# Kernel optimization log

Hardware: AMD Instinct MI355X
Metric: run time of the kernel (lower is better)

## Reference

```python
import jax, jax.numpy as jnp
import numpy as np

N = 32768      # total nodes
E = 524288     # edges (avg degree 16)
HID = 256      # hidden_dim
H = 8          # heads
C = HID // H   # head dim = 32
G = 64         # graphs in batch
NPG = N // G   # nodes per graph = 512
EDIM = 2       # edge feature dim
NEG_SLOPE = 0.2  # PyG GATv2 default


def setup_inputs():
    key = jax.random.key(0)
    ks = jax.random.split(key, 12)
    s = 0.05
    return dict(
        x=jax.random.normal(ks[0], (N, HID), jnp.float32),
        edge_attr=jax.random.normal(ks[1], (E, EDIM), jnp.float32),
        # GATv2Conv params
        W_l=jax.random.normal(ks[2], (HID, HID), jnp.float32) * s,
        b_l=jnp.zeros((HID,), jnp.float32),
        W_r=jax.random.normal(ks[3], (HID, HID), jnp.float32) * s,
        b_r=jnp.zeros((HID,), jnp.float32),
        W_e=jax.random.normal(ks[4], (EDIM, HID), jnp.float32) * s,
        att=jax.random.normal(ks[5], (H, C), jnp.float32) * s,
        bias_gat=jnp.zeros((HID,), jnp.float32),
        # MultiheadAttention params (torch packed qkv layout)
        in_proj_w=jax.random.normal(ks[6], (3 * HID, HID), jnp.float32) * s,
        in_proj_b=jnp.zeros((3 * HID,), jnp.float32),
        out_proj_w=jax.random.normal(ks[7], (HID, HID), jnp.float32) * s,
        out_proj_b=jnp.zeros((HID,), jnp.float32),
        alpha_param=jnp.array(0.5, jnp.float32),
        # FFN
        W1=jax.random.normal(ks[8], (HID, 4 * HID), jnp.float32) * s,
        b1=jnp.zeros((4 * HID,), jnp.float32),
        W2=jax.random.normal(ks[9], (4 * HID, HID), jnp.float32) * s,
        b2=jnp.zeros((HID,), jnp.float32),
        # LayerNorms
        g1=jnp.ones((HID,), jnp.float32), be1=jnp.zeros((HID,), jnp.float32),
        g2=jnp.ones((HID,), jnp.float32), be2=jnp.zeros((HID,), jnp.float32),
        g3=jnp.ones((HID,), jnp.float32), be3=jnp.zeros((HID,), jnp.float32),
        edge_index=jax.random.randint(ks[10], (2, E), 0, N, jnp.int32),
        batch=jnp.repeat(jnp.arange(G, dtype=jnp.int32), NPG),
    )


def _ln(x, g, b, eps=1e-5):
    m = jnp.mean(x, -1, keepdims=True)
    v = jnp.mean((x - m) ** 2, -1, keepdims=True)
    return (x - m) * jax.lax.rsqrt(v + eps) * g + b


def _gatv2(x, edge_index, edge_attr, W_l, b_l, W_r, b_r, W_e, att, bias_gat):
    src, dst = edge_index[0], edge_index[1]
    # PyG add_self_loops with fill_value='mean': self-loop edge_attr at node i
    # is the mean of edge_attr over edges incoming to i (0 if none).
    deg = jax.ops.segment_sum(jnp.ones((E,), x.dtype), dst, num_segments=N)
    ea_mean = jax.ops.segment_sum(edge_attr, dst, num_segments=N) / jnp.maximum(deg, 1.0)[:, None]
    loop = jnp.arange(N, dtype=src.dtype)
    src2 = jnp.concatenate([src, loop])
    dst2 = jnp.concatenate([dst, loop])
    ea2 = jnp.concatenate([edge_attr, ea_mean], axis=0)  # [E+N, 2]
    xl = (x @ W_l + b_l).reshape(N, H, C)  # source transform (messages)
    xr = (x @ W_r + b_r).reshape(N, H, C)  # target transform
    ee = (ea2 @ W_e).reshape(-1, H, C)
    e = jax.nn.leaky_relu(xl[src2] + xr[dst2] + ee, NEG_SLOPE)  # [E+N, H, C]
    score = jnp.einsum('ehc,hc->eh', e, att)  # [E+N, H]
    # scatter softmax over incoming edges of each target node
    smax = jax.lax.stop_gradient(jax.ops.segment_max(score, dst2, num_segments=N))
    ex = jnp.exp(score - smax[dst2])
    ssum = jax.ops.segment_sum(ex, dst2, num_segments=N)
    alpha = ex / ssum[dst2]  # [E+N, H]
    out = jax.ops.segment_sum(alpha[:, :, None] * xl[src2], dst2, num_segments=N)
    return out.reshape(N, HID) + bias_gat


def _mha(xg, in_proj_w, in_proj_b, out_proj_w, out_proj_b):
    # xg: [G, NPG, HID]; torch nn.MultiheadAttention (batch_first, eval mode)
    qkv = xg @ in_proj_w.T + in_proj_b
    q, k, v = jnp.split(qkv, 3, axis=-1)
    q = q.reshape(G, NPG, H, C)
    k = k.reshape(G, NPG, H, C)
    v = v.reshape(G, NPG, H, C)
    scores = jnp.einsum('gqhd,gkhd->ghqk', q, k) / jnp.sqrt(jnp.float32(C))
    p = jax.nn.softmax(scores, axis=-1)
    o = jnp.einsum('ghqk,gkhd->gqhd', p, v).reshape(G, NPG, HID)
    return o @ out_proj_w.T + out_proj_b


def reference(x, edge_attr, W_l, b_l, W_r, b_r, W_e, att, bias_gat,
              in_proj_w, in_proj_b, out_proj_w, out_proj_b, alpha_param,
              W1, b1, W2, b2, g1, be1, g2, be2, g3, be3, edge_index, batch):
    local_out = _ln(
        _gatv2(x, edge_index, edge_attr, W_l, b_l, W_r, b_r, W_e, att, bias_gat),
        g1, be1)
    # batch is sorted with equal-sized graphs -> the per-graph ragged
    # attention loop equals one batched [G, NPG, NPG] attention
    xg = x.reshape(G, NPG, HID)
    global_out = _mha(xg, in_proj_w, in_proj_b, out_proj_w, out_proj_b).reshape(N, HID)
    global_out = _ln(global_out, g2, be2)
    a = jax.nn.sigmoid(alpha_param)
    combined = a * local_out + (1.0 - a) * global_out
    ffn = jax.nn.gelu(combined @ W1 + b1, approximate=False) @ W2 + b2
    return _ln(combined + ffn, g3, be3)
```

## Files before the change

kernel.cpp:

```cpp
#include <hip/hip_runtime.h>
#include <math.h>

#define N_NODES 32768
#define E_EDGES 524288
#define HIDDEN  256
#define NPG     512
#define NGRAPH  64
#define NHEAD   8
#define CDIM    32

typedef unsigned short bf16;
typedef __attribute__((ext_vector_type(8))) short short8;
typedef __attribute__((ext_vector_type(4))) float f4;

__device__ inline float bf2f(unsigned short u) {
    union { unsigned int i; float f; } v; v.i = ((unsigned int)u) << 16; return v.f;
}
__device__ inline unsigned short f2bf(float f) {
    union { float f; unsigned int i; } v; v.f = f;
    unsigned int x = v.i;
    return (unsigned short)((x + 0x7FFFu + ((x >> 16) & 1u)) >> 16);
}
__device__ inline float4 load4(const float* p) { return *(const float4*)p; }
__device__ inline float4 load4(const bf16* p) {
    ushort4 u = *(const ushort4*)p;
    return make_float4(bf2f(u.x), bf2f(u.y), bf2f(u.z), bf2f(u.w));
}
__device__ inline void store4(float* p, float4 v) { *(float4*)p = v; }
__device__ inline void store4(bf16* p, float4 v) {
    ushort4 u; u.x = f2bf(v.x); u.y = f2bf(v.y); u.z = f2bf(v.z); u.w = f2bf(v.w);
    *(ushort4*)p = u;
}


__global__ void zero_kernel(float* deg, float* ea_sum, int* fill) {
    int i = blockIdx.x * blockDim.x + threadIdx.x;
    if (i < 2 * N_NODES) ea_sum[i] = 0.0f;
    if (i < N_NODES) { deg[i] = 0.0f; fill[i] = 0; }
}

__global__ void deg_kernel(const int* __restrict__ ei, const float* __restrict__ edge_attr,
                           float* deg, float* ea_sum) {
    int e = blockIdx.x * blockDim.x + threadIdx.x;
    if (e >= E_EDGES) return;
    int d = ei[E_EDGES + e];
    atomicAdd(&deg[d], 1.0f);
    atomicAdd(&ea_sum[2 * d + 0], edge_attr[2 * e + 0]);
    atomicAdd(&ea_sum[2 * d + 1], edge_attr[2 * e + 1]);
}

__global__ void eamean_kernel(const float* __restrict__ deg, float* ea_mean) {
    int i = blockIdx.x * blockDim.x + threadIdx.x;
    if (i >= N_NODES) return;
    float dm = fmaxf(deg[i], 1.0f);
    ea_mean[2 * i + 0] /= dm;
    ea_mean[2 * i + 1] /= dm;
}

__global__ __launch_bounds__(1024) void scan_kernel(const float* __restrict__ deg, int* row_ptr) {
    __shared__ int part[1024];
    int t = threadIdx.x;
    int base = t * 32;
    int loc[32];
    int s = 0;
    #pragma unroll
    for (int j = 0; j < 32; j++) {
        loc[j] = s;
        s += (int)deg[base + j] + 1;
    }
    int mysum = s;
    part[t] = s;
    __syncthreads();
    for (int off = 1; off < 1024; off <<= 1) {
        int v = 0;
        if (t >= off) v = part[t - off];
        __syncthreads();
        part[t] += v;
        __syncthreads();
    }
    int offset = part[t] - mysum;
    #pragma unroll
    for (int j = 0; j < 32; j++) row_ptr[base + j] = offset + loc[j];
    if (t == 1023) row_ptr[N_NODES] = part[1023];
}

__global__ void fill_kernel(const int* __restrict__ ei, const int* __restrict__ row_ptr,
                            int* fill, int* col) {
    int tid = blockIdx.x * blockDim.x + threadIdx.x;
    if (tid >= E_EDGES + N_NODES) return;
    int d;
    if (tid < E_EDGES) d = ei[E_EDGES + tid];
    else               d = tid - E_EDGES;
    int pos = row_ptr[d] + atomicAdd(&fill[d], 1);
    col[pos] = tid;
}

__global__ void convw_t(const float* __restrict__ src, bf16* __restrict__ dst, int K, int N) {
    int i = blockIdx.x * 256 + threadIdx.x;
    if (i >= K * N) return;
    int k = i / N, n = i - k * N;
    dst[n * K + k] = f2bf(src[i]);
}
__global__ void convv(const float* __restrict__ src, bf16* __restrict__ dst, int total4) {
    int i = blockIdx.x * 256 + threadIdx.x;
    if (i >= total4) return;
    float4 v = *(const float4*)&src[i * 4];
    store4(&dst[i * 4], v);
}

template <int EPI>
__global__ __launch_bounds__(256) void mfma_gemm(
    const bf16* __restrict__ A, const bf16* __restrict__ Wb,
    const float* __restrict__ bias, const bf16* __restrict__ res,
    bf16* __restrict__ C, int M, int N, int K)
{
    __shared__ bf16 lds[2 * 128 * 72];
    bf16* As = lds;
    bf16* Bs = lds + 128 * 72;
    int tid = threadIdx.x;
    int wave = tid >> 6, lane = tid & 63;
    int quad = lane >> 4, l16 = lane & 15;
    int n0 = blockIdx.x * 128, m0 = blockIdx.y * 128;
    int wm = (wave & 1) * 64, wn = (wave >> 1) * 64;

    f4 acc[4][4] = {};

    for (int k0 = 0; k0 < K; k0 += 64) {
        #pragma unroll
        for (int i = 0; i < 4; i++) {
            int idx = i * 256 + tid;
            int row = idx >> 3, kc = (idx & 7) * 8;
            *(int4*)&As[row * 72 + kc] = *(const int4*)&A[(size_t)(m0 + row) * K + k0 + kc];
            *(int4*)&Bs[row * 72 + kc] = *(const int4*)&Wb[(size_t)(n0 + row) * K + k0 + kc];
        }
        __syncthreads();
        #pragma unroll
        for (int ks = 0; ks < 2; ks++) {
            short8 af[4], bfr[4];
            #pragma unroll
            for (int mt = 0; mt < 4; mt++)
                af[mt] = *(const short8*)&As[(wm + mt * 16 + l16) * 72 + ks * 32 + quad * 8];
            #pragma unroll
            for (int nt = 0; nt < 4; nt++)
                bfr[nt] = *(const short8*)&Bs[(wn + nt * 16 + l16) * 72 + ks * 32 + quad * 8];
            #pragma unroll
            for (int mt = 0; mt < 4; mt++)
                #pragma unroll
                for (int nt = 0; nt < 4; nt++)
                    acc[mt][nt] = __builtin_amdgcn_mfma_f32_16x16x32_bf16(
                        af[mt], bfr[nt], acc[mt][nt], 0, 0, 0);
        }
        __syncthreads();
    }

    float* epi = (float*)lds + wave * 16 * 68;
    int row = lane >> 2;
    int cb = (lane & 3) * 16;
    int gn = n0 + wn + cb;
    float bb[16];
    *(float4*)&bb[0]  = *(const float4*)&bias[gn + 0];
    *(float4*)&bb[4]  = *(const float4*)&bias[gn + 4];
    *(float4*)&bb[8]  = *(const float4*)&bias[gn + 8];
    *(float4*)&bb[12] = *(const float4*)&bias[gn + 12];

    for (int mt = 0; mt < 4; mt++) {
        #pragma unroll
        for (int nt = 0; nt < 4; nt++)
            #pragma unroll
            for (int r = 0; r < 4; r++)
                epi[(quad * 4 + r) * 68 + nt * 16 + l16] = acc[mt][nt][r];
        float vv[16];
        *(float4*)&vv[0]  = *(float4*)&epi[row * 68 + cb + 0];
        *(float4*)&vv[4]  = *(float4*)&epi[row * 68 + cb + 4];
        *(float4*)&vv[8]  = *(float4*)&epi[row * 68 + cb + 8];
        *(float4*)&vv[12] = *(float4*)&epi[row * 68 + cb + 12];
        int gm = m0 + wm + mt * 16 + row;
        #pragma unroll
        for (int j = 0; j < 16; j++) vv[j] += bb[j];
        if (EPI == 1) {
            #pragma unroll
            for (int j = 0; j < 16; j++)
                vv[j] = 0.5f * vv[j] * (1.0f + erff(vv[j] * 0.70710678118654752f));
        } else if (EPI == 2) {
            ushort rr[16];
            const bf16* rp = &res[(size_t)gm * N + gn];
            *(int4*)&rr[0] = *(const int4*)&rp[0];
            *(int4*)&rr[8] = *(const int4*)&rp[8];
            #pragma unroll
            for (int j = 0; j < 16; j++) vv[j] += bf2f(rr[j]);
        }
        ushort o16[16];
        #pragma unroll
        for (int j = 0; j < 16; j++) o16[j] = f2bf(vv[j]);
        bf16* cp = &C[(size_t)gm * N + gn];
        *(int4*)&cp[0] = *(int4*)&o16[0];
        *(int4*)&cp[8] = *(int4*)&o16[8];
    }
}

__global__ __launch_bounds__(256) void attn_mfma(
    const bf16* __restrict__ qkv, bf16* __restrict__ attnout)
{
    __shared__ bf16 Ks[128 * 40];
    __shared__ bf16 Vt[32 * 136];
    __shared__ bf16 Pb[4 * 64 * 40];

    int b = blockIdx.x;
    int g = b >> 4, h = (b >> 1) & 7, hlf = b & 1;
    int tid = threadIdx.x;
    int wave = tid >> 6, lane = tid & 63;
    int quad = lane >> 4, l16 = lane & 15;
    int qbase = hlf * 256 + wave * 64;
    bf16* Pw = &Pb[wave * 64 * 40];
    const float SCALE = 0.17677669529663687f;

    short8 qf[4];
    #pragma unroll
    for (int mt = 0; mt < 4; mt++) {
        size_t node = (size_t)(g * NPG + qbase + mt * 16 + l16);
        qf[mt] = *(const short8*)&qkv[node * 768 + h * CDIM + quad * 8];
    }

    f4 oacc[4][2] = {};
    float lacc[4][4] = {};

    for (int c = 0; c < 4; c++) {
        int kk0 = c * 128;
        __syncthreads();
        #pragma unroll
        for (int i = 0; i < 2; i++) {
            int idx = i * 256 + tid;
            int key = idx >> 2, kc = (idx & 3) * 8;
            *(int4*)&Ks[key * 40 + kc] =
                *(const int4*)&qkv[(size_t)(g * NPG + kk0 + key) * 768 + 256 + h * CDIM + kc];
        }
        {
            int key = tid >> 1, dblk = (tid & 1) * 16;
            ushort tmp[16];
            const bf16* vp = &qkv[(size_t)(g * NPG + kk0 + key) * 768 + 512 + h * CDIM + dblk];
            *(int4*)&tmp[0] = *(const int4*)&vp[0];
            *(int4*)&tmp[8] = *(const int4*)&vp[8];
            #pragma unroll
            for (int j = 0; j < 16; j++) Vt[(dblk + j) * 136 + key] = tmp[j];
        }
        __syncthreads();

        for (int sub = 0; sub < 4; sub++) {
            int ks0 = sub * 32;
            short8 kf[2];
            #pragma unroll
            for (int nt = 0; nt < 2; nt++)
                kf[nt] = *(const short8*)&Ks[(ks0 + nt * 16 + l16) * 40 + quad * 8];
            #pragma unroll
            for (int mt = 0; mt < 4; mt++) {
                #pragma unroll
                for (int nt = 0; nt < 2; nt++) {
                    f4 z = {0.f, 0.f, 0.f, 0.f};
                    f4 s = __builtin_amdgcn_mfma_f32_16x16x32_bf16(qf[mt], kf[nt], z, 0, 0, 0);
                    #pragma unroll
                    for (int r = 0; r < 4; r++) {
                        float p = __expf(s[r] * SCALE);
                        lacc[mt][r] += p;
                        Pw[(mt * 16 + quad * 4 + r) * 40 + nt * 16 + l16] = f2bf(p);
                    }
                }
            }
            short8 vf[2];
            #pragma unroll
            for (int dt = 0; dt < 2; dt++)
                vf[dt] = *(const short8*)&Vt[(dt * 16 + l16) * 136 + ks0 + quad * 8];
            #pragma unroll
            for (int mt = 0; mt < 4; mt++) {
                short8 pf = *(const short8*)&Pw[(mt * 16 + l16) * 40 + quad * 8];
                #pragma unroll
                for (int dt = 0; dt < 2; dt++)
                    oacc[mt][dt] = __builtin_amdgcn_mfma_f32_16x16x32_bf16(
                        pf, vf[dt], oacc[mt][dt], 0, 0, 0);
            }
        }
    }

    #pragma unroll
    for (int mt = 0; mt < 4; mt++)
        #pragma unroll
        for (int r = 0; r < 4; r++) {
            float l = lacc[mt][r];
            l += __shfl_xor(l, 1);
            l += __shfl_xor(l, 2);
            l += __shfl_xor(l, 4);
            l += __shfl_xor(l, 8);
            lacc[mt][r] = l;
        }

    #pragma unroll
    for (int mt = 0; mt < 4; mt++) {
        #pragma unroll
        for (int dt = 0; dt < 2; dt++) {
            #pragma unroll
            for (int r = 0; r < 4; r++) {
                float v = oacc[mt][dt][r] / lacc[mt][r];
                size_t node = (size_t)(g * NPG + qbase + mt * 16 + quad * 4 + r);
                attnout[node * HIDDEN + h * CDIM + dt * 16 + l16] = f2bf(v);
            }
        }
    }
}

__global__ __launch_bounds__(256) void gat_kernel(
    const bf16* __restrict__ xl, const bf16* __restrict__ xr,
    const int* __restrict__ row_ptr, const int* __restrict__ col,
    const int* __restrict__ ei, const float* __restrict__ edge_attr,
    const float* __restrict__ ea_mean,
    const float* __restrict__ W_e, const float* __restrict__ att,
    const float* __restrict__ bias_gat,
    const float* __restrict__ g1, const float* __restrict__ be1,
    bf16* __restrict__ out)
{
    int wave = threadIdx.x >> 6;
    int lane = threadIdx.x & 63;
    int node = blockIdx.x * 4 + wave;
    int cb = lane * 4;

    float4 xr4 = load4(&xr[(size_t)node * HIDDEN + cb]);
    float4 we0 = *(const float4*)&W_e[cb];
    float4 we1 = *(const float4*)&W_e[HIDDEN + cb];
    float4 at4 = *(const float4*)&att[cb];

    int rs = row_ptr[node], re = row_ptr[node + 1];
    float lsum = 0.0f;
    float acc0 = 0.f, acc1 = 0.f, acc2 = 0.f, acc3 = 0.f;

    for (int idx = rs; idx < re; idx++) {
        int eid = col[idx];
        int s; float ea0, ea1;
        if (eid < E_EDGES) {
            s = ei[eid];
            ea0 = edge_attr[2 * eid + 0];
            ea1 = edge_attr[2 * eid + 1];
        } else {
            s = node;
            ea0 = ea_mean[2 * node + 0];
            ea1 = ea_mean[2 * node + 1];
        }
        float4 xl4 = load4(&xl[(size_t)s * HIDDEN + cb]);
        float t, p = 0.0f;
        t = xl4.x + xr4.x + ea0 * we0.x + ea1 * we1.x; t = (t > 0.f) ? t : 0.2f * t; p += t * at4.x;
        t = xl4.y + xr4.y + ea0 * we0.y + ea1 * we1.y; t = (t > 0.f) ? t : 0.2f * t; p += t * at4.y;
        t = xl4.z + xr4.z + ea0 * we0.z + ea1 * we1.z; t = (t > 0.f) ? t : 0.2f * t; p += t * at4.z;
        t = xl4.w + xr4.w + ea0 * we0.w + ea1 * we1.w; t = (t > 0.f) ? t : 0.2f * t; p += t * at4.w;
        p += __shfl_xor(p, 1);
        p += __shfl_xor(p, 2);
        p += __shfl_xor(p, 4);
        float w = __expf(p);
        lsum += w;
        acc0 += w * xl4.x; acc1 += w * xl4.y; acc2 += w * xl4.z; acc3 += w * xl4.w;
    }
    float inv = 1.0f / lsum;
    float v0 = acc0 * inv + bias_gat[cb + 0];
    float v1 = acc1 * inv + bias_gat[cb + 1];
    float v2 = acc2 * inv + bias_gat[cb + 2];
    float v3 = acc3 * inv + bias_gat[cb + 3];

    float s = v0 + v1 + v2 + v3;
    #pragma unroll
    for (int m = 1; m < 64; m <<= 1) s += __shfl_xor(s, m);
    float mean = s * (1.0f / 256.0f);
    float d0 = v0 - mean, d1 = v1 - mean, d2 = v2 - mean, d3 = v3 - mean;
    float sq = d0 * d0 + d1 * d1 + d2 * d2 + d3 * d3;
    #pragma unroll
    for (int m = 1; m < 64; m <<= 1) sq += __shfl_xor(sq, m);
    float rstd = rsqrtf(sq * (1.0f / 256.0f) + 1e-5f);
    float4 o;
    o.x = d0 * rstd * g1[cb + 0] + be1[cb + 0];
    o.y = d1 * rstd * g1[cb + 1] + be1[cb + 1];
    o.z = d2 * rstd * g1[cb + 2] + be1[cb + 2];
    o.w = d3 * rstd * g1[cb + 3] + be1[cb + 3];
    store4(&out[(size_t)node * HIDDEN + cb], o);
}

__global__ __launch_bounds__(256) void combine_kernel(
    const bf16* __restrict__ gout, const bf16* __restrict__ localout,
    const float* __restrict__ alpha_p,
    const float* __restrict__ g2, const float* __restrict__ be2,
    bf16* __restrict__ combined)
{
    int wave = threadIdx.x >> 6;
    int lane = threadIdx.x & 63;
    int node = blockIdx.x * 4 + wave;
    int cb = lane * 4;
    float4 gv = load4(&gout[(size_t)node * HIDDEN + cb]);
    float s = gv.x + gv.y + gv.z + gv.w;
    #pragma unroll
    for (int m = 1; m < 64; m <<= 1) s += __shfl_xor(s, m);
    float mean = s * (1.0f / 256.0f);
    float d0 = gv.x - mean, d1 = gv.y - mean, d2 = gv.z - mean, d3 = gv.w - mean;
    float sq = d0 * d0 + d1 * d1 + d2 * d2 + d3 * d3;
    #pragma unroll
    for (int m = 1; m < 64; m <<= 1) sq += __shfl_xor(sq, m);
    float rstd = rsqrtf(sq * (1.0f / 256.0f) + 1e-5f);
    float n0 = d0 * rstd * g2[cb + 0] + be2[cb + 0];
    float n1 = d1 * rstd * g2[cb + 1] + be2[cb + 1];
    float n2 = d2 * rstd * g2[cb + 2] + be2[cb + 2];
    float n3 = d3 * rstd * g2[cb + 3] + be2[cb + 3];
    float a = 1.0f / (1.0f + __expf(-alpha_p[0]));
    float4 lv = load4(&localout[(size_t)node * HIDDEN + cb]);
    float4 o;
    o.x = a * lv.x + (1.0f - a) * n0;
    o.y = a * lv.y + (1.0f - a) * n1;
    o.z = a * lv.z + (1.0f - a) * n2;
    o.w = a * lv.w + (1.0f - a) * n3;
    store4(&combined[(size_t)node * HIDDEN + cb], o);
}

__global__ __launch_bounds__(256) void finalln_kernel(
    const bf16* __restrict__ ffn,
    const float* __restrict__ g3, const float* __restrict__ be3,
    float* __restrict__ out)
{
    int wave = threadIdx.x >> 6;
    int lane = threadIdx.x & 63;
    int node = blockIdx.x * 4 + wave;
    int cb = lane * 4;
    float4 v = load4(&ffn[(size_t)node * HIDDEN + cb]);
    float s = v.x + v.y + v.z + v.w;
    #pragma unroll
    for (int m = 1; m < 64; m <<= 1) s += __shfl_xor(s, m);
    float mean = s * (1.0f / 256.0f);
    float d0 = v.x - mean, d1 = v.y - mean, d2 = v.z - mean, d3 = v.w - mean;
    float sq = d0 * d0 + d1 * d1 + d2 * d2 + d3 * d3;
    #pragma unroll
    for (int m = 1; m < 64; m <<= 1) sq += __shfl_xor(sq, m);
    float rstd = rsqrtf(sq * (1.0f / 256.0f) + 1e-5f);
    float4 o;
    o.x = d0 * rstd * g3[cb + 0] + be3[cb + 0];
    o.y = d1 * rstd * g3[cb + 1] + be3[cb + 1];
    o.z = d2 * rstd * g3[cb + 2] + be3[cb + 2];
    o.w = d3 * rstd * g3[cb + 3] + be3[cb + 3];
    *(float4*)&out[(size_t)node * HIDDEN + cb] = o;
}

extern "C" void kernel_launch(void* const* d_in, const int* in_sizes, int n_in,
                              void* d_out, int out_size, void* d_ws, size_t ws_size,
                              hipStream_t stream) {
    const float* x          = (const float*)d_in[0];
    const float* edge_attr  = (const float*)d_in[1];
    const float* W_l        = (const float*)d_in[2];
    const float* b_l        = (const float*)d_in[3];
    const float* W_r        = (const float*)d_in[4];
    const float* b_r        = (const float*)d_in[5];
    const float* W_e        = (const float*)d_in[6];
    const float* att        = (const float*)d_in[7];
    const float* bias_gat   = (const float*)d_in[8];
    const float* in_proj_w  = (const float*)d_in[9];
    const float* in_proj_b  = (const float*)d_in[10];
    const float* out_proj_w = (const float*)d_in[11];
    const float* out_proj_b = (const float*)d_in[12];
    const float* alpha_p    = (const float*)d_in[13];
    const float* W1         = (const float*)d_in[14];
    const float* b1         = (const float*)d_in[15];
    const float* W2         = (const float*)d_in[16];
    const float* b2         = (const float*)d_in[17];
    const float* g1  = (const float*)d_in[18];
    const float* be1 = (const float*)d_in[19];
    const float* g2  = (const float*)d_in[20];
    const float* be2 = (const float*)d_in[21];
    const float* g3  = (const float*)d_in[22];
    const float* be3 = (const float*)d_in[23];
    const int* edge_index = (const int*)d_in[24];

    char* base = (char*)d_ws;
    const size_t MB = 1024 * 1024;
    float* deg     = (float*)(base + 0);
    float* ea_mean = (float*)(base + 131072);
    int*   fill    = (int*)  (base + 393216);
    int*   row_ptr = (int*)  (base + 524288);
    int*   col     = (int*)  (base + 786432);
    bf16* wlb  = (bf16*)(base + 3 * MB);
    bf16* wrb  = (bf16*)(base + 3 * MB + 512 * 1024);
    bf16* wipb = (bf16*)(base + 4 * MB);
    bf16* wopb = (bf16*)(base + 4 * MB + 512 * 1024);
    bf16* w1b  = (bf16*)(base + 5 * MB);
    bf16* w2b  = (bf16*)(base + 5 * MB + 512 * 1024);
    bf16* xb       = (bf16*)(base + 8 * MB);
    bf16* qkv      = (bf16*)(base + 24 * MB);
    bf16* attnout  = (bf16*)(base + 72 * MB);
    bf16* gout     = (bf16*)(base + 24 * MB);
    bf16* xl       = (bf16*)(base + 40 * MB);
    bf16* xr       = (bf16*)(base + 56 * MB);
    bf16* localout = (bf16*)(base + 72 * MB);
    bf16* combined = (bf16*)(base + 8 * MB);
    bf16* h1h      = (bf16*)(base + 24 * MB);
    bf16* ffn      = (bf16*)(base + 56 * MB);
    float* out = (float*)d_out;

    zero_kernel<<<(2 * N_NODES + 255) / 256, 256, 0, stream>>>(deg, ea_mean, fill);
    deg_kernel<<<E_EDGES / 256, 256, 0, stream>>>(edge_index, edge_attr, deg, ea_mean);
    eamean_kernel<<<N_NODES / 256, 256, 0, stream>>>(deg, ea_mean);
    scan_kernel<<<1, 1024, 0, stream>>>(deg, row_ptr);
    fill_kernel<<<(E_EDGES + N_NODES) / 256, 256, 0, stream>>>(edge_index, row_ptr, fill, col);

    convw_t<<<256, 256, 0, stream>>>(W_l, wlb, 256, 256);
    convw_t<<<256, 256, 0, stream>>>(W_r, wrb, 256, 256);
    convw_t<<<1024, 256, 0, stream>>>(W1, w1b, 256, 1024);
    convw_t<<<1024, 256, 0, stream>>>(W2, w2b, 1024, 256);
    convv<<<192, 256, 0, stream>>>(in_proj_w, wipb, 49152);
    convv<<<64, 256, 0, stream>>>(out_proj_w, wopb, 16384);
    convv<<<8192, 256, 0, stream>>>(x, xb, 2097152);

    mfma_gemm<0><<<dim3(768 / 128, N_NODES / 128), 256, 0, stream>>>(
        xb, wipb, in_proj_b, (const bf16*)nullptr, qkv, N_NODES, 768, 256);
    attn_mfma<<<NGRAPH * NHEAD * 2, 256, 0, stream>>>(qkv, attnout);
    mfma_gemm<0><<<dim3(256 / 128, N_NODES / 128), 256, 0, stream>>>(
        attnout, wopb, out_proj_b, (const bf16*)nullptr, gout, N_NODES, 256, 256);

    mfma_gemm<0><<<dim3(256 / 128, N_NODES / 128), 256, 0, stream>>>(
        xb, wlb, b_l, (const bf16*)nullptr, xl, N_NODES, 256, 256);
    mfma_gemm<0><<<dim3(256 / 128, N_NODES / 128), 256, 0, stream>>>(
        xb, wrb, b_r, (const bf16*)nullptr, xr, N_NODES, 256, 256);
    gat_kernel<<<N_NODES / 4, 256, 0, stream>>>(
        xl, xr, row_ptr, col, edge_index, edge_attr, ea_mean,
        W_e, att, bias_gat, g1, be1, localout);

    combine_kernel<<<N_NODES / 4, 256, 0, stream>>>(
        gout, localout, alpha_p, g2, be2, combined);

    for (int hh = 0; hh < 2; hh++) {
        const bf16* ch = combined + (size_t)hh * 16384 * 256;
        bf16* fh = ffn + (size_t)hh * 16384 * 256;
        mfma_gemm<1><<<dim3(1024 / 128, 16384 / 128), 256, 0, stream>>>(
            ch, w1b, b1, (const bf16*)nullptr, h1h, 16384, 1024, 256);
        mfma_gemm<2><<<dim3(256 / 128, 16384 / 128), 256, 0, stream>>>(
            h1h, w2b, b2, ch, fh, 16384, 256, 1024);
    }

    finalln_kernel<<<N_NODES / 4, 256, 0, stream>>>(ffn, g3, be3, out);
}
```

Baseline: 630.7 us.

## Fuse weight conversions, merge W_l/W_r GEMM, use global_load_lds, split GAT edges

All fp32-to-bf16 conversion launches are merged into one kernel, and W_l and W_r are concatenated so a single N=512 GEMM produces xl and xr together. The GEMM staging now uses global_load_lds direct-to-LDS copies with an unpadded 64-wide row instead of register round-trips into a padded layout. The GAT kernel splits each node's edge list across two waves with software-prefetched metadata and reduces the two halves through LDS. Together these aim to cut launch overhead, extra passes over x, and gather latency. The unpadded LDS layout may add bank conflicts on the fragment reads.

```diff
diff --git a/kernel.cpp b/kernel.cpp
--- a/kernel.cpp
+++ b/kernel.cpp
@@ -12,6 +12,14 @@
 typedef unsigned short bf16;
 typedef __attribute__((ext_vector_type(8))) short short8;
 typedef __attribute__((ext_vector_type(4))) float f4;
+
+#define AS1 __attribute__((address_space(1)))
+#define AS3 __attribute__((address_space(3)))
+
+__device__ __forceinline__ void cp16(const bf16* g, bf16* l) {
+    __builtin_amdgcn_global_load_lds((AS1 const unsigned int*)(const void*)g,
+                                     (AS3 unsigned int*)(void*)l, 16, 0, 0);
+}
 
 __device__ inline float bf2f(unsigned short u) {
     union { unsigned int i; float f; } v; v.i = ((unsigned int)u) << 16; return v.f;
@@ -95,17 +103,39 @@
     col[pos] = tid;
 }
 
-__global__ void convw_t(const float* __restrict__ src, bf16* __restrict__ dst, int K, int N) {
-    int i = blockIdx.x * 256 + threadIdx.x;
-    if (i >= K * N) return;
-    int k = i / N, n = i - k * N;
-    dst[n * K + k] = f2bf(src[i]);
-}
-__global__ void convv(const float* __restrict__ src, bf16* __restrict__ dst, int total4) {
-    int i = blockIdx.x * 256 + threadIdx.x;
-    if (i >= total4) return;
-    float4 v = *(const float4*)&src[i * 4];
-    store4(&dst[i * 4], v);
+__global__ void convall(const float* __restrict__ x,
+                        const float* __restrict__ W_l, const float* __restrict__ W_r,
+                        const float* __restrict__ W1, const float* __restrict__ W2,
+                        const float* __restrict__ in_proj_w, const float* __restrict__ out_proj_w,
+                        const float* __restrict__ b_l, const float* __restrict__ b_r,
+                        bf16* xb, bf16* wlrb, bf16* w1b, bf16* w2b,
+                        bf16* wipb, bf16* wopb, float* blr)
+{
+    int b = blockIdx.x, t = threadIdx.x;
+    if (b < 8192) {
+        int i = b * 256 + t;
+        store4(&xb[i * 4], *(const float4*)&x[i * 4]);
+    } else if (b < 8448) {
+        int i = (b - 8192) * 256 + t; int k = i >> 8, n = i & 255;
+        wlrb[n * 256 + k] = f2bf(W_l[i]);
+    } else if (b < 8704) {
+        int i = (b - 8448) * 256 + t; int k = i >> 8, n = i & 255;
+        wlrb[(256 + n) * 256 + k] = f2bf(W_r[i]);
+    } else if (b < 9728) {
+        int i = (b - 8704) * 256 + t; int k = i >> 10, n = i & 1023;
+        w1b[n * 256 + k] = f2bf(W1[i]);
+    } else if (b < 10752) {
+        int i = (b - 9728) * 256 + t; int k = i >> 8, n = i & 255;
+        w2b[n * 1024 + k] = f2bf(W2[i]);
+    } else if (b < 10944) {
+        int i = (b - 10752) * 256 + t;
+        store4(&wipb[i * 4], *(const float4*)&in_proj_w[i * 4]);
+    } else if (b < 11008) {
+        int i = (b - 10944) * 256 + t;
+        store4(&wopb[i * 4], *(const float4*)&out_proj_w[i * 4]);
+    } else {
+        blr[t] = b_l[t]; blr[256 + t] = b_r[t];
+    }
 }
 
 template <int EPI>
@@ -114,9 +144,9 @@
     const float* __restrict__ bias, const bf16* __restrict__ res,
     bf16* __restrict__ C, int M, int N, int K)
 {
-    __shared__ bf16 lds[2 * 128 * 72];
+    __shared__ bf16 lds[2 * 128 * 64];
     bf16* As = lds;
-    bf16* Bs = lds + 128 * 72;
+    bf16* Bs = lds + 128 * 64;
     int tid = threadIdx.x;
     int wave = tid >> 6, lane = tid & 63;
     int quad = lane >> 4, l16 = lane & 15;
@@ -125,13 +155,15 @@
 
     f4 acc[4][4] = {};
 
+    int srow = tid >> 3;
+    int scol = (tid & 7) * 8;
+
     for (int k0 = 0; k0 < K; k0 += 64) {
         #pragma unroll
         for (int i = 0; i < 4; i++) {
-            int idx = i * 256 + tid;
-            int row = idx >> 3, kc = (idx & 7) * 8;
-            *(int4*)&As[row * 72 + kc] = *(const int4*)&A[(size_t)(m0 + row) * K + k0 + kc];
-            *(int4*)&Bs[row * 72 + kc] = *(const int4*)&Wb[(size_t)(n0 + row) * K + k0 + kc];
+            int row = i * 32 + srow;
+            cp16(&A[(size_t)(m0 + row) * K + k0 + scol], &As[row * 64 + scol]);
+            cp16(&Wb[(size_t)(n0 + row) * K + k0 + scol], &Bs[row * 64 + scol]);
         }
         __syncthreads();
         #pragma unroll
@@ -139,10 +171,10 @@
             short8 af[4], bfr[4];
             #pragma unroll
             for (int mt = 0; mt < 4; mt++)
-                af[mt] = *(const short8*)&As[(wm + mt * 16 + l16) * 72 + ks * 32 + quad * 8];
+                af[mt] = *(const short8*)&As[(wm + mt * 16 + l16) * 64 + ks * 32 + quad * 8];
             #pragma unroll
             for (int nt = 0; nt < 4; nt++)
-                bfr[nt] = *(const short8*)&Bs[(wn + nt * 16 + l16) * 72 + ks * 32 + quad * 8];
+                bfr[nt] = *(const short8*)&Bs[(wn + nt * 16 + l16) * 64 + ks * 32 + quad * 8];
             #pragma unroll
             for (int mt = 0; mt < 4; mt++)
                 #pragma unroll
@@ -306,8 +338,25 @@
     }
 }
 
+__device__ __forceinline__ void fetchmeta(
+    int i, int re, int node, const int* __restrict__ col, const int* __restrict__ ei,
+    const float* __restrict__ edge_attr, const float* __restrict__ ea_mean,
+    int& s, float& a0, float& a1)
+{
+    if (i < re) {
+        int e = col[i];
+        if (e < E_EDGES) {
+            s = ei[e]; a0 = edge_attr[2 * e]; a1 = edge_attr[2 * e + 1];
+        } else {
+            s = node; a0 = ea_mean[2 * node]; a1 = ea_mean[2 * node + 1];
+        }
+    } else {
+        s = node; a0 = 0.f; a1 = 0.f;
+    }
+}
+
 __global__ __launch_bounds__(256) void gat_kernel(
-    const bf16* __restrict__ xl, const bf16* __restrict__ xr,
+    const bf16* __restrict__ xlr,
     const int* __restrict__ row_ptr, const int* __restrict__ col,
     const int* __restrict__ ei, const float* __restrict__ edge_attr,
     const float* __restrict__ ea_mean,
@@ -316,66 +365,85 @@
     const float* __restrict__ g1, const float* __restrict__ be1,
     bf16* __restrict__ out)
 {
+    __shared__ float pacc[2][260];
+    __shared__ float plsum[2][64];
     int wave = threadIdx.x >> 6;
     int lane = threadIdx.x & 63;
-    int node = blockIdx.x * 4 + wave;
+    int nloc = wave >> 1, half = wave & 1;
+    int node = blockIdx.x * 2 + nloc;
     int cb = lane * 4;
 
-    float4 xr4 = load4(&xr[(size_t)node * HIDDEN + cb]);
+    float4 xr4 = load4(&xlr[(size_t)node * 512 + 256 + cb]);
     float4 we0 = *(const float4*)&W_e[cb];
     float4 we1 = *(const float4*)&W_e[HIDDEN + cb];
     float4 at4 = *(const float4*)&att[cb];
 
     int rs = row_ptr[node], re = row_ptr[node + 1];
-    float lsum = 0.0f;
+
+    float lsum = 0.f;
     float acc0 = 0.f, acc1 = 0.f, acc2 = 0.f, acc3 = 0.f;
 
-    for (int idx = rs; idx < re; idx++) {
-        int eid = col[idx];
-        int s; float ea0, ea1;
-        if (eid < E_EDGES) {
-            s = ei[eid];
-            ea0 = edge_attr[2 * eid + 0];
-            ea1 = edge_attr[2 * eid + 1];
-        } else {
-            s = node;
-            ea0 = ea_mean[2 * node + 0];
-            ea1 = ea_mean[2 * node + 1];
-        }
-        float4 xl4 = load4(&xl[(size_t)s * HIDDEN + cb]);
-        float t, p = 0.0f;
-        t = xl4.x + xr4.x + ea0 * we0.x + ea1 * we1.x; t = (t > 0.f) ? t : 0.2f * t; p += t * at4.x;
-        t = xl4.y + xr4.y + ea0 * we0.y + ea1 * we1.y; t = (t > 0.f) ? t : 0.2f * t; p += t * at4.y;
-        t = xl4.z + xr4.z + ea0 * we0.z + ea1 * we1.z; t = (t > 0.f) ? t : 0.2f * t; p += t * at4.z;
-        t = xl4.w + xr4.w + ea0 * we0.w + ea1 * we1.w; t = (t > 0.f) ? t : 0.2f * t; p += t * at4.w;
+    int i0 = rs + half;
+    int s0, s1; float a00, a01, a10, a11;
+    fetchmeta(i0,     re, node, col, ei, edge_attr, ea_mean, s0, a00, a01);
+    fetchmeta(i0 + 2, re, node, col, ei, edge_attr, ea_mean, s1, a10, a11);
+    ushort4 xu0 = *(const ushort4*)&xlr[(size_t)s0 * 512 + cb];
+
+    for (int i = i0; i < re; i += 2) {
+        int s2; float a20, a21;
+        fetchmeta(i + 4, re, node, col, ei, edge_attr, ea_mean, s2, a20, a21);
+        ushort4 xu1 = *(const ushort4*)&xlr[(size_t)s1 * 512 + cb];
+
+        float4 xl4 = make_float4(bf2f(xu0.x), bf2f(xu0.y), bf2f(xu0.z), bf2f(xu0.w));
+        float t, p = 0.f;
+        t = xl4.x + xr4.x + a00 * we0.x + a01 * we1.x; t = (t > 0.f) ? t : 0.2f * t; p += t * at4.x;
+        t = xl4.y + xr4.y + a00 * we0.y + a01 * we1.y; t = (t > 0.f) ? t : 0.2f * t; p += t * at4.y;
+        t = xl4.z + xr4.z + a00 * we0.z + a01 * we1.z; t = (t > 0.f) ? t : 0.2f * t; p += t * at4.z;
+        t = xl4.w + xr4.w + a00 * we0.w + a01 * we1.w; t = (t > 0.f) ? t : 0.2f * t; p += t * at4.w;
         p += __shfl_xor(p, 1);
         p += __shfl_xor(p, 2);
         p += __shfl_xor(p, 4);
         float w = __expf(p);
         lsum += w;
         acc0 += w * xl4.x; acc1 += w * xl4.y; acc2 += w * xl4.z; acc3 += w * xl4.w;
-    }
-    float inv = 1.0f / lsum;
-    float v0 = acc0 * inv + bias_gat[cb + 0];
-    float v1 = acc1 * inv + bias_gat[cb + 1];
-    float v2 = acc2 * inv + bias_gat[cb + 2];
-    float v3 = acc3 * inv + bias_gat[cb + 3];
-
-    float s = v0 + v1 + v2 + v3;
-    #pragma unroll
-    for (int m = 1; m < 64; m <<= 1) s += __shfl_xor(s, m);
-    float mean = s * (1.0f / 256.0f);
-    float d0 = v0 - mean, d1 = v1 - mean, d2 = v2 - mean, d3 = v3 - mean;
-    float sq = d0 * d0 + d1 * d1 + d2 * d2 + d3 * d3;
-    #pragma unroll
-    for (int m = 1; m < 64; m <<= 1) sq += __shfl_xor(sq, m);
-    float rstd = rsqrtf(sq * (1.0f / 256.0f) + 1e-5f);
-    float4 o;
-    o.x = d0 * rstd * g1[cb + 0] + be1[cb + 0];
-    o.y = d1 * rstd * g1[cb + 1] + be1[cb + 1];
-    o.z = d2 * rstd * g1[cb + 2] + be1[cb + 2];
-    o.w = d3 * rstd * g1[cb + 3] + be1[cb + 3];
-    store4(&out[(size_t)node * HIDDEN + cb], o);
+
+        s0 = s1; a00 = a10; a01 = a11; xu0 = xu1;
+        s1 = s2; a10 = a20; a11 = a21;
+    }
+
+    if (half) {
+        plsum[nloc][lane] = lsum;
+        pacc[nloc][cb + 0] = acc0; pacc[nloc][cb + 1] = acc1;
+        pacc[nloc][cb + 2] = acc2; pacc[nloc][cb + 3] = acc3;
+    }
+    __syncthreads();
+    if (!half) {
+        lsum += plsum[nloc][lane];
+        acc0 += pacc[nloc][cb + 0]; acc1 += pacc[nloc][cb + 1];
+        acc2 += pacc[nloc][cb + 2]; acc3 += pacc[nloc][cb + 3];
+
+        float inv = 1.0f / lsum;
+        float v0 = acc0 * inv + bias_gat[cb + 0];
+        float v1 = acc1 * inv + bias_gat[cb + 1];
+        float v2 = acc2 * inv + bias_gat[cb + 2];
+        float v3 = acc3 * inv + bias_gat[cb + 3];
+
+        float s = v0 + v1 + v2 + v3;
+        #pragma unroll
+        for (int m = 1; m < 64; m <<= 1) s += __shfl_xor(s, m);
+        float mean = s * (1.0f / 256.0f);
+        float d0 = v0 - mean, d1 = v1 - mean, d2 = v2 - mean, d3 = v3 - mean;
+        float sq = d0 * d0 + d1 * d1 + d2 * d2 + d3 * d3;
+        #pragma unroll
+        for (int m = 1; m < 64; m <<= 1) sq += __shfl_xor(sq, m);
+        float rstd = rsqrtf(sq * (1.0f / 256.0f) + 1e-5f);
+        float4 o;
+        o.x = d0 * rstd * g1[cb + 0] + be1[cb + 0];
+        o.y = d1 * rstd * g1[cb + 1] + be1[cb + 1];
+        o.z = d2 * rstd * g1[cb + 2] + be1[cb + 2];
+        o.w = d3 * rstd * g1[cb + 3] + be1[cb + 3];
+        store4(&out[(size_t)node * HIDDEN + cb], o);
+    }
 }
 
 __global__ __launch_bounds__(256) void combine_kernel(
@@ -470,23 +538,23 @@
 
     char* base = (char*)d_ws;
     const size_t MB = 1024 * 1024;
+    const size_t KB = 1024;
     float* deg     = (float*)(base + 0);
     float* ea_mean = (float*)(base + 131072);
     int*   fill    = (int*)  (base + 393216);
     int*   row_ptr = (int*)  (base + 524288);
     int*   col     = (int*)  (base + 786432);
-    bf16* wlb  = (bf16*)(base + 3 * MB);
-    bf16* wrb  = (bf16*)(base + 3 * MB + 512 * 1024);
-    bf16* wipb = (bf16*)(base + 4 * MB);
-    bf16* wopb = (bf16*)(base + 4 * MB + 512 * 1024);
-    bf16* w1b  = (bf16*)(base + 5 * MB);
-    bf16* w2b  = (bf16*)(base + 5 * MB + 512 * 1024);
+    bf16* wlrb = (bf16*)(base + 3 * MB);
+    bf16* wipb = (bf16*)(base + 3 * MB + 256 * KB);
+    bf16* wopb = (bf16*)(base + 3 * MB + 640 * KB);
+    bf16* w1b  = (bf16*)(base + 3 * MB + 768 * KB);
+    bf16* w2b  = (bf16*)(base + 3 * MB + 1280 * KB);
+    float* blr = (float*)(base + 5 * MB);
     bf16* xb       = (bf16*)(base + 8 * MB);
     bf16* qkv      = (bf16*)(base + 24 * MB);
     bf16* attnout  = (bf16*)(base + 72 * MB);
     bf16* gout     = (bf16*)(base + 24 * MB);
-    bf16* xl       = (bf16*)(base + 40 * MB);
-    bf16* xr       = (bf16*)(base + 56 * MB);
+    bf16* xlr      = (bf16*)(base + 40 * MB);
     bf16* localout = (bf16*)(base + 72 * MB);
     bf16* combined = (bf16*)(base + 8 * MB);
     bf16* h1h      = (bf16*)(base + 24 * MB);
@@ -499,26 +567,19 @@
     scan_kernel<<<1, 1024, 0, stream>>>(deg, row_ptr);
     fill_kernel<<<(E_EDGES + N_NODES) / 256, 256, 0, stream>>>(edge_index, row_ptr, fill, col);
 
-    convw_t<<<256, 256, 0, stream>>>(W_l, wlb, 256, 256);
-    convw_t<<<256, 256, 0, stream>>>(W_r, wrb, 256, 256);
-    convw_t<<<1024, 256, 0, stream>>>(W1, w1b, 256, 1024);
-    convw_t<<<1024, 256, 0, stream>>>(W2, w2b, 1024, 256);
-    convv<<<192, 256, 0, stream>>>(in_proj_w, wipb, 49152);
-    convv<<<64, 256, 0, stream>>>(out_proj_w, wopb, 16384);
-    convv<<<8192, 256, 0, stream>>>(x, xb, 2097152);
-
-    mfma_gemm<0><<<dim3(768 / 128, N_NODES / 128), 256, 0, stream>>>(
+    convall<<<11009, 256, 0, stream>>>(x, W_l, W_r, W1, W2, in_proj_w, out_proj_w,
+                                       b_l, b_r, xb, wlrb, w1b, w2b, wipb, wopb, blr);
+
+    mfma_gemm<0><<<dim3(6, 256), 256, 0, stream>>>(
         xb, wipb, in_proj_b, (const bf16*)nullptr, qkv, N_NODES, 768, 256);
     attn_mfma<<<NGRAPH * NHEAD * 2, 256, 0, stream>>>(qkv, attnout);
-    mfma_gemm<0><<<dim3(256 / 128, N_NODES / 128), 256, 0, stream>>>(
+    mfma_gemm<0><<<dim3(2, 256), 256, 0, stream>>>(
         attnout, wopb, out_proj_b, (const bf16*)nullptr, gout, N_NODES, 256, 256);
 
-    mfma_gemm<0><<<dim3(256 / 128, N_NODES / 128), 256, 0, stream>>>(
-        xb, wlb, b_l, (const bf16*)nullptr, xl, N_NODES, 256, 256);
-    mfma_gemm<0><<<dim3(256 / 128, N_NODES / 128), 256, 0, stream>>>(
-        xb, wrb, b_r, (const bf16*)nullptr, xr, N_NODES, 256, 256);
-    gat_kernel<<<N_NODES / 4, 256, 0, stream>>>(
-        xl, xr, row_ptr, col, edge_index, edge_attr, ea_mean,
+    mfma_gemm<0><<<dim3(4, 256), 256, 0, stream>>>(
+        xb, wlrb, blr, (const bf16*)nullptr, xlr, N_NODES, 512, 256);
+    gat_kernel<<<N_NODES / 2, 256, 0, stream>>>(
+        xlr, row_ptr, col, edge_index, edge_attr, ea_mean,
         W_e, att, bias_gat, g1, be1, localout);
 
     combine_kernel<<<N_NODES / 4, 256, 0, stream>>>(
@@ -527,9 +588,9 @@
     for (int hh = 0; hh < 2; hh++) {
         const bf16* ch = combined + (size_t)hh * 16384 * 256;
         bf16* fh = ffn + (size_t)hh * 16384 * 256;
-        mfma_gemm<1><<<dim3(1024 / 128, 16384 / 128), 256, 0, stream>>>(
+        mfma_gemm<1><<<dim3(8, 128), 256, 0, stream>>>(
             ch, w1b, b1, (const bf16*)nullptr, h1h, 16384, 1024, 256);
-        mfma_gemm<2><<<dim3(256 / 128, 16384 / 128), 256, 0, stream>>>(
+        mfma_gemm<2><<<dim3(2, 128), 256, 0, stream>>>(
             h1h, w2b, b2, ch, fh, 16384, 256, 1024);
     }
 
```

Measured after the change: 609.6 us. 3.3% less time.
